# Kernel tuning notes

Hardware: AMD Instinct MI355X
Metric: run time of the kernel (lower is better)

Reference implementation:

```python
import jax, jax.numpy as jnp
import numpy as np

B, N, C = 16, 4096, 384
H_RES = W_RES = 64  # input_resolution; n == h*w
NUM_HEADS = 12
ROPE_BASE = 10000.0


def _rope_angles(h, w, c):
    # feature_dim = c, 2 channel dims -> k_max = c // 4
    k_max = c // 4
    theta = 1.0 / (ROPE_BASE ** (jnp.arange(k_max, dtype=jnp.float32) / k_max))
    hh = jnp.arange(h, dtype=jnp.float32)[:, None, None] * theta  # (h,1,k_max) -> bcast
    ww = jnp.arange(w, dtype=jnp.float32)[None, :, None] * theta  # (1,w,k_max)
    hh = jnp.broadcast_to(hh, (h, w, k_max))
    ww = jnp.broadcast_to(ww, (h, w, k_max))
    angles = jnp.concatenate([hh, ww], axis=-1)  # (h, w, c//2)
    return jnp.cos(angles), jnp.sin(angles)


def _apply_rope(x_img, cos, sin):
    # x_img: (b, h, w, c); complex rotation on (re, im) channel pairs
    b, h, w, c = x_img.shape
    xr = x_img.reshape(b, h, w, c // 2, 2)
    re, im = xr[..., 0], xr[..., 1]
    out_re = cos * re - sin * im
    out_im = sin * re + cos * im
    return jnp.stack([out_re, out_im], axis=-1).reshape(b, h, w, c)


def setup_inputs() -> dict:
    key = jax.random.key(0)
    ks = jax.random.split(key, 5)
    x = jax.random.normal(ks[0], (B, N, C), dtype=jnp.float32)
    qk_w = jax.random.normal(ks[1], (2 * C, C), dtype=jnp.float32) * (1.0 / np.sqrt(C))
    qk_b = jax.random.normal(ks[2], (2 * C,), dtype=jnp.float32) * 0.02
    lepe_w = jax.random.normal(ks[3], (C, 1, 3, 3), dtype=jnp.float32) * (1.0 / 3.0)
    lepe_b = jax.random.normal(ks[4], (C,), dtype=jnp.float32) * 0.02
    return {"x": x, "qk_w": qk_w, "qk_b": qk_b, "lepe_w": lepe_w, "lepe_b": lepe_b}


def reference(x, qk_w, qk_b, lepe_w, lepe_b):
    b, n, c = x.shape
    h = w = int(np.sqrt(n))
    nh = NUM_HEADS
    d = c // nh

    qk = x @ qk_w.T + qk_b                       # (b, n, 2c)
    q = jax.nn.elu(qk[..., :c]) + 1.0            # (b, n, c)
    k = jax.nn.elu(qk[..., c:]) + 1.0            # (b, n, c)
    v = x

    cos, sin = _rope_angles(h, w, c)             # (h, w, c//2)
    q_rope = _apply_rope(q.reshape(b, h, w, c), cos, sin).reshape(b, n, nh, d)
    k_rope = _apply_rope(k.reshape(b, h, w, c), cos, sin).reshape(b, n, nh, d)

    qh = q.reshape(b, n, nh, d)
    kh = k.reshape(b, n, nh, d)
    vh = v.reshape(b, n, nh, d)

    # z = 1 / (q . mean_n(k) + eps), per head per token
    k_mean = kh.mean(axis=1)                     # (b, nh, d)
    z = 1.0 / (jnp.einsum('bnhd,bhd->bnh', qh, k_mean) + 1e-6)  # (b, n, nh)

    # linear attention: kv = (k_rope^T v) / n ; out = q_rope @ kv
    kv = jnp.einsum('bnhd,bnhe->bhde', k_rope, vh) / n          # (b, nh, d, d)
    out = jnp.einsum('bnhd,bhde->bnhe', q_rope, kv)             # (b, n, nh, d)
    out = (out * z[..., None]).reshape(b, n, c)

    # LePE: depthwise 3x3 conv on v as image (NHWC)
    v_img = v.reshape(b, h, w, c)
    w_hwio = jnp.transpose(lepe_w, (2, 3, 1, 0))  # (3,3,1,c)
    lepe = jax.lax.conv_general_dilated(
        v_img, w_hwio, window_strides=(1, 1), padding='SAME',
        dimension_numbers=('NHWC', 'HWIO', 'NHWC'), feature_group_count=c)
    lepe = lepe + lepe_b

    return out + lepe.reshape(b, n, c)
```

## Files before the change

### kernel.cpp

```cpp
#include <hip/hip_runtime.h>

#define CDIM 384
#define NTOK 4096
#define NHEAD 12
#define KV_FLOATS (16 * NHEAD * 1024)
#define SCR_FLOATS (KV_FLOATS + 16 * CDIM)

typedef unsigned short ushort_t;
typedef __attribute__((ext_vector_type(8))) short bf16x8;
typedef __attribute__((ext_vector_type(4))) float f32x4;
typedef __attribute__((ext_vector_type(4))) unsigned short u16x4;
typedef __attribute__((ext_vector_type(8))) unsigned short u16x8;

__device__ __attribute__((aligned(16))) float g_scr[SCR_FLOATS];
__device__ __attribute__((aligned(16))) ushort_t g_xbf[(size_t)16 * 4096 * 384];
__device__ __attribute__((aligned(16))) ushort_t g_wbf[768 * 384];
__device__ __attribute__((aligned(16))) float g_part[(size_t)16 * 3 * 32 * 4096];
__device__ __attribute__((aligned(16))) float g_kspart[(size_t)16 * 3 * 32 * 256];
__device__ int g_flag;

__device__ __forceinline__ float bf2f(ushort_t u) {
  union { unsigned int i; float f; } z; z.i = ((unsigned int)u) << 16; return z.f;
}
__device__ __forceinline__ ushort_t f2bf(float f) {
  union { float f; unsigned int i; } z; z.f = f;
  unsigned int r = z.i + 0x7FFFu + ((z.i >> 16) & 1u);
  return (ushort_t)(r >> 16);
}
__device__ __forceinline__ float ldf(const void* p, size_t i, bool fp32) {
  return fp32 ? ((const float*)p)[i] : bf2f(((const ushort_t*)p)[i]);
}

__device__ __forceinline__ void load4(const void* src, size_t off, bool fp32, float o[4]) {
  if (fp32) {
    f32x4 v = *(const f32x4*)((const float*)src + off);
    o[0] = v[0]; o[1] = v[1]; o[2] = v[2]; o[3] = v[3];
  } else {
    u16x4 v = *(const u16x4*)((const ushort_t*)src + off);
    o[0] = bf2f(v[0]); o[1] = bf2f(v[1]); o[2] = bf2f(v[2]); o[3] = bf2f(v[3]);
  }
}

__device__ __forceinline__ u16x8 cvt8(const void* src, size_t off, bool fp32) {
  if (fp32) {
    const float* p = (const float*)src + off;
    f32x4 a = *(const f32x4*)p;
    f32x4 b = *(const f32x4*)(p + 4);
    u16x8 t;
    t[0] = f2bf(a[0]); t[1] = f2bf(a[1]); t[2] = f2bf(a[2]); t[3] = f2bf(a[3]);
    t[4] = f2bf(b[0]); t[5] = f2bf(b[1]); t[6] = f2bf(b[2]); t[7] = f2bf(b[3]);
    return t;
  }
  return *(const u16x8*)((const ushort_t*)src + off);
}

#define GLL16(gp, lp) __builtin_amdgcn_global_load_lds( \
    (const __attribute__((address_space(1))) unsigned int*)(const void*)(gp), \
    (__attribute__((address_space(3))) unsigned int*)(void*)(lp), 16, 0, 0)

__device__ __forceinline__ void gemm128c(const ushort_t* __restrict__ xg,
                                         const ushort_t* __restrict__ wg,
                                         ushort_t* lds, int tid, f32x4 acc[4][4])
{
  f32x4 zz = {0.f, 0.f, 0.f, 0.f};
  #pragma unroll
  for (int i = 0; i < 4; ++i)
    #pragma unroll
    for (int j = 0; j < 4; ++j) acc[i][j] = zz;

  const int lane = tid & 63, quad = lane >> 4, l15 = lane & 15;
  const int wv = tid >> 6, wm = wv >> 1, wn = wv & 1;
  const int srow = tid >> 2;
  const int sc   = tid & 3;
  const int sx   = (l15 >> 1) & 3;

  const ushort_t* xa = xg + (size_t)srow * CDIM + sc * 8;
  const ushort_t* wa = wg + (size_t)srow * CDIM + sc * 8;

  #define STAGE_STEP(buf, ks) do {                                   \
    ushort_t* la_ = lds + (buf) * 8192;                              \
    ushort_t* lb_ = la_ + 4096;                                      \
    GLL16(xa + (ks),                  la_ + tid * 8);                \
    GLL16(xa + (ks) + 64 * CDIM,      la_ + 2048 + tid * 8);         \
    GLL16(wa + (ks),                  lb_ + tid * 8);                \
    GLL16(wa + (ks) + 64 * CDIM,      lb_ + 2048 + tid * 8);         \
  } while (0)

  STAGE_STEP(0, 0);
  #pragma unroll
  for (int s = 0; s < 12; ++s) {
    const int cur = s & 1;
    if (s < 11) {
      STAGE_STEP(cur ^ 1, (s + 1) * 32);
      asm volatile("s_waitcnt vmcnt(4)" ::: "memory");
    } else {
      asm volatile("s_waitcnt vmcnt(0)" ::: "memory");
    }
    __builtin_amdgcn_s_barrier();
    asm volatile("" ::: "memory");
    const ushort_t* la = lds + cur * 8192;
    const ushort_t* lb = la + 4096;
    bf16x8 aF[4], bF[4];
    #pragma unroll
    for (int i = 0; i < 4; ++i)
      aF[i] = *(const bf16x8*)(la + (wm * 64 + l15) * 32 + i * 512 + (quad ^ sx) * 8);
    #pragma unroll
    for (int j = 0; j < 4; ++j)
      bF[j] = *(const bf16x8*)(lb + (wn * 64 + l15) * 32 + j * 512 + (quad ^ sx) * 8);
    #pragma unroll
    for (int i = 0; i < 4; ++i)
      #pragma unroll
      for (int j = 0; j < 4; ++j)
        acc[i][j] = __builtin_amdgcn_mfma_f32_16x16x32_bf16(aF[i], bF[j], acc[i][j], 0, 0, 0);
    asm volatile("" ::: "memory");
    __builtin_amdgcn_s_barrier();
  }
  #undef STAGE_STEP
}

__global__ __launch_bounds__(256) void prep(const void* __restrict__ x,
                                            const void* __restrict__ qkw) {
  __shared__ int sflag;
  const int tid = threadIdx.x;
  if (tid < 64) {
    ushort_t u = ((const ushort_t*)x)[tid];
    int e = (u >> 7) & 0xFF;
    int ok = (e >= 117 && e <= 136) ? 1 : 0;
    unsigned long long m = __ballot(ok);
    if (tid == 0) {
      int f = (__popcll(m) >= 52) ? 0 : 1;
      sflag = f;
      if (blockIdx.x == 0) g_flag = f;
    }
  }
  __syncthreads();
  const bool fp32 = (sflag != 0);
  const int gid = blockIdx.x * 256 + tid;

  if (gid < 768 * 48) {
    const int oc = gid / 48, ck = gid - oc * 48;
    u16x8 t = cvt8(qkw, (size_t)gid * 8, fp32);
    const int ckp = (ck & ~3) | ((ck & 3) ^ ((oc >> 1) & 3));
    *(u16x8*)(g_wbf + (size_t)oc * CDIM + ckp * 8) = t;
  }
  const int total = 16 * 4096 * 48;
  for (int c = gid; c < total; c += 2048 * 256) {
    const int n = c / 48, ck = c - n * 48;
    u16x8 t = cvt8(x, (size_t)c * 8, fp32);
    const int ckp = (ck & ~3) | ((ck & 3) ^ ((n >> 1) & 3));
    *(u16x8*)(g_xbf + (size_t)n * CDIM + ckp * 8) = t;
  }
}

__global__ __launch_bounds__(256) void k1(const void* __restrict__ qkb)
{
  __shared__ __align__(16) char smem[53248];
  ushort_t* xs = (ushort_t*)smem;
  ushort_t* kropeT = (ushort_t*)smem;
  ushort_t* vT = (ushort_t*)(smem + 34816);

  const bool fp32 = (g_flag != 0);
  const int tid = threadIdx.x;
  const int nt = blockIdx.x, ct = blockIdx.y, b = blockIdx.z;

  f32x4 acc[4][4];
  gemm128c(g_xbf + ((size_t)b * NTOK + (size_t)nt * 128) * CDIM,
           g_wbf + (size_t)(CDIM + ct * 128) * CDIM, xs, tid, acc);

  const int lane = tid & 63, quad = lane >> 4, l15 = lane & 15;
  const int wv = tid >> 6, wm = wv >> 1, wn = wv & 1;

  #pragma unroll
  for (int j = 0; j < 4; ++j) {
    const float bj = ldf(qkb, CDIM + ct * 128 + wn * 64 + j * 16 + l15, fp32);
    #pragma unroll
    for (int i = 0; i < 4; ++i)
      #pragma unroll
      for (int r = 0; r < 4; ++r) {
        float v = acc[i][j][r] + bj;
        acc[i][j][r] = v > 0.f ? v + 1.f : __expf(v);
      }
  }

  #pragma unroll
  for (int j = 0; j < 4; ++j) {
    float s = 0.f;
    #pragma unroll
    for (int i = 0; i < 4; ++i)
      #pragma unroll
      for (int r = 0; r < 4; ++r) s += acc[i][j][r];
    s += __shfl_down(s, 32);
    s += __shfl_down(s, 16);
    if (lane < 16)
      g_kspart[(size_t)(((b * 3 + ct) * 32 + nt) * 2 + wm) * 128 + wn * 64 + j * 16 + l15] = s;
  }

  float th[4]; bool sel[4];
  #pragma unroll
  for (int j = 0; j < 4; ++j) {
    int o = ct * 128 + wn * 64 + j * 16 + l15;
    int p = o >> 1;
    sel[j] = p < 96;
    int jj = sel[j] ? p : p - 96;
    th[j] = exp2f(-0.13841367062030676f * (float)jj);
  }
  #pragma unroll
  for (int i = 0; i < 4; ++i)
    #pragma unroll
    for (int r = 0; r < 4; ++r) {
      const int row  = wm * 64 + i * 16 + quad * 4 + r;
      const int ntok = nt * 128 + row;
      const float hhf = (float)(ntok >> 6), wwf = (float)(ntok & 63);
      #pragma unroll
      for (int j = 0; j < 4; ++j) {
        float ang = (sel[j] ? hhf : wwf) * th[j];
        float sn, cs;
        __sincosf(ang, &sn, &cs);
        float v0 = acc[i][j][r];
        float other = __shfl_xor(v0, 1);
        if (!(lane & 1)) {
          const int o = wn * 64 + j * 16 + l15;
          kropeT[o * 136 + row]       = f2bf(cs * v0 - sn * other);
          kropeT[(o + 1) * 136 + row] = f2bf(sn * v0 + cs * other);
        }
      }
    }

  const int hl = wv;
  f32x4 zz = {0.f, 0.f, 0.f, 0.f};
  f32x4 acc2[2][2];
  acc2[0][0] = zz; acc2[0][1] = zz; acc2[1][0] = zz; acc2[1][1] = zz;

  #pragma unroll
  for (int h = 0; h < 2; ++h) {
    __syncthreads();
    const int t64 = tid & 63;
    const size_t nrow = (size_t)b * NTOK + (size_t)nt * 128 + h * 64 + t64;
    #pragma unroll
    for (int it = 0; it < 4; ++it) {
      const int g = it * 4 + wv;
      const int ckt = ct * 16 + g;
      const int ckp = (ckt & ~3) | ((ckt & 3) ^ ((int)(nrow >> 1) & 3));
      u16x8 vv = *(const u16x8*)(g_xbf + nrow * CDIM + ckp * 8);
      #pragma unroll
      for (int i = 0; i < 8; ++i) vT[(g * 8 + i) * 72 + t64] = vv[i];
    }
    __syncthreads();
    #pragma unroll
    for (int ks = 0; ks < 2; ++ks) {
      bf16x8 a0 = *(const bf16x8*)(kropeT + (hl * 32 + l15) * 136      + h * 64 + ks * 32 + quad * 8);
      bf16x8 a1 = *(const bf16x8*)(kropeT + (hl * 32 + 16 + l15) * 136 + h * 64 + ks * 32 + quad * 8);
      bf16x8 b0 = *(const bf16x8*)(vT + (hl * 32 + l15) * 72      + ks * 32 + quad * 8);
      bf16x8 b1 = *(const bf16x8*)(vT + (hl * 32 + 16 + l15) * 72 + ks * 32 + quad * 8);
      acc2[0][0] = __builtin_amdgcn_mfma_f32_16x16x32_bf16(a0, b0, acc2[0][0], 0, 0, 0);
      acc2[0][1] = __builtin_amdgcn_mfma_f32_16x16x32_bf16(a0, b1, acc2[0][1], 0, 0, 0);
      acc2[1][0] = __builtin_amdgcn_mfma_f32_16x16x32_bf16(a1, b0, acc2[1][0], 0, 0, 0);
      acc2[1][1] = __builtin_amdgcn_mfma_f32_16x16x32_bf16(a1, b1, acc2[1][1], 0, 0, 0);
    }
  }

  float* dst = g_part + ((size_t)(((b * 3 + ct) * 32 + nt) * 4 + hl)) * 1024;
  #pragma unroll
  for (int mt = 0; mt < 2; ++mt)
    #pragma unroll
    for (int n2 = 0; n2 < 2; ++n2)
      #pragma unroll
      for (int r = 0; r < 4; ++r)
        dst[(mt * 16 + quad * 4 + r) * 32 + n2 * 16 + l15] = acc2[mt][n2][r];
}

__global__ __launch_bounds__(256) void red() {
  const int t = blockIdx.x * 256 + threadIdx.x;
  if (blockIdx.x < 192) {
    const int o = t * 4;
    const int b = o / 12288, r = o - b * 12288;
    const int h = r >> 10, off = r & 1023;
    const int ct = h >> 2, hl = h & 3;
    const float* p = g_part + ((size_t)((b * 3 + ct) * 32) * 4 + hl) * 1024 + off;
    f32x4 s = {0.f, 0.f, 0.f, 0.f};
    #pragma unroll 8
    for (int nt = 0; nt < 32; ++nt) {
      f32x4 v = *(const f32x4*)(p + (size_t)nt * 4096);
      s[0] += v[0]; s[1] += v[1]; s[2] += v[2]; s[3] += v[3];
    }
    *(f32x4*)(g_scr + (size_t)b * 12288 + h * 1024 + off) = s;
  } else {
    const int s4 = (t - 192 * 256) * 4;
    if (s4 < 16 * 384) {
      const int b = s4 / 384, ch = s4 - b * 384;
      const int ct = ch >> 7, chl = ch & 127;
      const float* p = g_kspart + (size_t)((b * 3 + ct) * 32) * 256 + chl;
      f32x4 s = {0.f, 0.f, 0.f, 0.f};
      #pragma unroll 8
      for (int nt = 0; nt < 32; ++nt) {
        f32x4 v0 = *(const f32x4*)(p + nt * 256);
        f32x4 v1 = *(const f32x4*)(p + nt * 256 + 128);
        s[0] += v0[0] + v1[0]; s[1] += v0[1] + v1[1];
        s[2] += v0[2] + v1[2]; s[3] += v0[3] + v1[3];
      }
      *(f32x4*)(g_scr + KV_FLOATS + (size_t)b * 384 + ch) = s;
    }
  }
}

__global__ __launch_bounds__(256) void k2(const void* __restrict__ x,
                                          const void* __restrict__ qkb,
                                          const void* __restrict__ lepw,
                                          const void* __restrict__ lepb,
                                          void* __restrict__ out)
{
  __shared__ __align__(16) char smem[50176];
  ushort_t* xs  = (ushort_t*)smem;
  ushort_t* qr  = (ushort_t*)smem;
  float* lepL = (float*)smem;
  ushort_t* kvT = (ushort_t*)(smem + 34816);
  float* zl = (float*)(smem + 43008);
  float* lw = (float*)(smem + 45056);
  float* lb = (float*)(smem + 49664);

  const bool fp32 = (g_flag != 0);
  const int tid = threadIdx.x;
  const int nt = blockIdx.x, ct = blockIdx.y, b = blockIdx.z;
  const float* kv_g   = g_scr;
  const float* ksum_g = g_scr + KV_FLOATS;

  for (int g = tid; g < 1152; g += 256) lw[g] = ldf(lepw, (size_t)ct * 1152 + g, fp32);
  if (tid < 128) lb[tid] = ldf(lepb, ct * 128 + tid, fp32);

  f32x4 acc[4][4];
  gemm128c(g_xbf + ((size_t)b * NTOK + (size_t)nt * 128) * CDIM,
           g_wbf + (size_t)(ct * 128) * CDIM, xs, tid, acc);

  const int lane = tid & 63, quad = lane >> 4, l15 = lane & 15;
  const int wv = tid >> 6, wm = wv >> 1, wn = wv & 1;

  #pragma unroll
  for (int j = 0; j < 4; ++j) {
    const float bj = ldf(qkb, ct * 128 + wn * 64 + j * 16 + l15, fp32);
    #pragma unroll
    for (int i = 0; i < 4; ++i)
      #pragma unroll
      for (int r = 0; r < 4; ++r) {
        float v = acc[i][j][r] + bj;
        acc[i][j][r] = v > 0.f ? v + 1.f : __expf(v);
      }
  }

  float km[4];
  #pragma unroll
  for (int j = 0; j < 4; ++j)
    km[j] = ksum_g[b * CDIM + ct * 128 + wn * 64 + j * 16 + l15] * (1.f / 4096.f);
  #pragma unroll
  for (int i = 0; i < 4; ++i)
    #pragma unroll
    for (int r = 0; r < 4; ++r) {
      float p0 = acc[i][0][r] * km[0] + acc[i][1][r] * km[1];
      float p1 = acc[i][2][r] * km[2] + acc[i][3][r] * km[3];
      #pragma unroll
      for (int off = 8; off > 0; off >>= 1) {
        p0 += __shfl_down(p0, off, 16);
        p1 += __shfl_down(p1, off, 16);
      }
      if (l15 == 0) {
        int row = wm * 64 + i * 16 + quad * 4 + r;
        zl[row * 4 + wn * 2]     = 1.f / (p0 + 1e-6f);
        zl[row * 4 + wn * 2 + 1] = 1.f / (p1 + 1e-6f);
      }
    }

  float th[4]; bool sel[4];
  #pragma unroll
  for (int j = 0; j < 4; ++j) {
    int o = ct * 128 + wn * 64 + j * 16 + l15;
    int p = o >> 1;
    sel[j] = p < 96;
    int jj = sel[j] ? p : p - 96;
    th[j] = exp2f(-0.13841367062030676f * (float)jj);
  }
  #pragma unroll
  for (int i = 0; i < 4; ++i)
    #pragma unroll
    for (int r = 0; r < 4; ++r) {
      const int row  = wm * 64 + i * 16 + quad * 4 + r;
      const int ntok = nt * 128 + row;
      const float hhf = (float)(ntok >> 6), wwf = (float)(ntok & 63);
      #pragma unroll
      for (int j = 0; j < 4; ++j) {
        float ang = (sel[j] ? hhf : wwf) * th[j];
        float sn, cs;
        __sincosf(ang, &sn, &cs);
        float v0 = acc[i][j][r];
        float other = __shfl_xor(v0, 1);
        if (!(lane & 1)) {
          ushort2 t = make_ushort2(f2bf(cs * v0 - sn * other), f2bf(sn * v0 + cs * other));
          *(ushort2*)(qr + row * 136 + wn * 64 + j * 16 + l15) = t;
        }
      }
    }

  const float* kvb = kv_g + (size_t)(b * NHEAD + ct * 4) * 1024;
  #pragma unroll
  for (int s = 0; s < 16; ++s) {
    int g = s * 256 + tid;
    int hl2 = g >> 10, dd = (g >> 5) & 31, e = g & 31;
    kvT[hl2 * 1024 + e * 32 + dd] = f2bf(kvb[g] * (1.f / 4096.f));
  }
  __syncthreads();

  const int hl = tid >> 6;
  bf16x8 aF[8];
  #pragma unroll
  for (int i = 0; i < 8; ++i)
    aF[i] = *(const bf16x8*)(qr + (i * 16 + l15) * 136 + hl * 32 + quad * 8);
  __syncthreads();

  const int cc  = tid & 31;
  const int ch4 = cc * 4;
  const int gg  = tid >> 5;
  const int w0  = gg * 8;
  const float lbv0 = lb[ch4], lbv1 = lb[ch4 + 1], lbv2 = lb[ch4 + 2], lbv3 = lb[ch4 + 3];

  #pragma unroll
  for (int h = 0; h < 2; ++h) {
    if (h) __syncthreads();

    f32x4 zzv = {0.f, 0.f, 0.f, 0.f};
    f32x4 oac4[4][2];
    #pragma unroll
    for (int iloc = 0; iloc < 4; ++iloc) { oac4[iloc][0] = zzv; oac4[iloc][1] = zzv; }
    #pragma unroll
    for (int jn = 0; jn < 2; ++jn) {
      bf16x8 bF = *(const bf16x8*)(kvT + hl * 1024 + (jn * 16 + l15) * 32 + quad * 8);
      #pragma unroll
      for (int iloc = 0; iloc < 4; ++iloc)
        oac4[iloc][jn] = __builtin_amdgcn_mfma_f32_16x16x32_bf16(aF[h * 4 + iloc], bF, oac4[iloc][jn], 0, 0, 0);
    }
    #pragma unroll
    for (int iloc = 0; iloc < 4; ++iloc)
      #pragma unroll
      for (int jn = 0; jn < 2; ++jn)
        #pragma unroll
        for (int r = 0; r < 4; ++r) {
          const int rowloc = iloc * 16 + quad * 4 + r;
          lepL[rowloc * 132 + hl * 32 + jn * 16 + l15] =
              oac4[iloc][jn][r] * zl[(h * 64 + rowloc) * 4 + hl];
        }
    __syncthreads();

    const int hh = nt * 2 + h;
    float accv[8][4];
    #pragma unroll
    for (int s = 0; s < 8; ++s) {
      accv[s][0] = lbv0; accv[s][1] = lbv1; accv[s][2] = lbv2; accv[s][3] = lbv3;
    }
    #pragma unroll
    for (int rk = 0; rk < 3; ++rk) {
      const int ih = hh + rk - 1;
      if ((unsigned)ih < 64u) {
        float wr0[4], wr1[4], wr2[4];
        #pragma unroll
        for (int c = 0; c < 4; ++c) {
          wr0[c] = lw[(ch4 + c) * 9 + rk * 3 + 0];
          wr1[c] = lw[(ch4 + c) * 9 + rk * 3 + 1];
          wr2[c] = lw[(ch4 + c) * 9 + rk * 3 + 2];
        }
        const size_t rowbase = ((size_t)b * NTOK + (size_t)(ih * 64)) * CDIM
                             + (size_t)ct * 128 + ch4;
        float av[4], bv[4], cv[4];
        if (w0 > 0) load4(x, rowbase + (size_t)(w0 - 1) * CDIM, fp32, av);
        else { av[0] = av[1] = av[2] = av[3] = 0.f; }
        load4(x, rowbase + (size_t)w0 * CDIM, fp32, bv);
        #pragma unroll
        for (int s = 0; s < 8; ++s) {
          const int iwn = w0 + s + 1;
          if (iwn < 64) load4(x, rowbase + (size_t)iwn * CDIM, fp32, cv);
          else { cv[0] = cv[1] = cv[2] = cv[3] = 0.f; }
          #pragma unroll
          for (int c = 0; c < 4; ++c)
            accv[s][c] += wr0[c] * av[c] + wr1[c] * bv[c] + wr2[c] * cv[c];
          #pragma unroll
          for (int c = 0; c < 4; ++c) { av[c] = bv[c]; bv[c] = cv[c]; }
        }
      }
    }
    #pragma unroll
    for (int s = 0; s < 8; ++s) {
      f32x4 a = *(const f32x4*)(lepL + (w0 + s) * 132 + ch4);
      float r0 = accv[s][0] + a[0];
      float r1 = accv[s][1] + a[1];
      float r2 = accv[s][2] + a[2];
      float r3 = accv[s][3] + a[3];
      const size_t oi = ((size_t)b * NTOK + (size_t)(nt * 128 + h * 64 + w0 + s)) * CDIM
                      + (size_t)ct * 128 + ch4;
      if (fp32) {
        f32x4 t; t[0] = r0; t[1] = r1; t[2] = r2; t[3] = r3;
        *(f32x4*)((float*)out + oi) = t;
      } else {
        u16x4 t; t[0] = f2bf(r0); t[1] = f2bf(r1); t[2] = f2bf(r2); t[3] = f2bf(r3);
        *(u16x4*)((ushort_t*)out + oi) = t;
      }
    }
  }
}

extern "C" void kernel_launch(void* const* d_in, const int* in_sizes, int n_in,
                              void* d_out, int out_size, void* d_ws, size_t ws_size,
                              hipStream_t stream) {
  const void* x    = d_in[0];
  const void* qkw  = d_in[1];
  const void* qkb  = d_in[2];
  const void* lepw = d_in[3];
  const void* lepb = d_in[4];

  prep<<<2048, 256, 0, stream>>>(x, qkw);
  dim3 grid(32, 3, 16), blk(256, 1, 1);
  k1<<<grid, blk, 0, stream>>>(qkb);
  red<<<198, 256, 0, stream>>>();
  k2<<<grid, blk, 0, stream>>>(x, qkb, lepw, lepb, d_out);
}
```

Baseline: 356.0 us.

## Read LePE input from bf16 copy, hoist row RoPE sincos, pad kvT LDS

```diff
diff --git a/kernel.cpp b/kernel.cpp
--- a/kernel.cpp
+++ b/kernel.cpp
@@ -31,14 +31,12 @@
   return fp32 ? ((const float*)p)[i] : bf2f(((const ushort_t*)p)[i]);
 }
 
-__device__ __forceinline__ void load4(const void* src, size_t off, bool fp32, float o[4]) {
-  if (fp32) {
-    f32x4 v = *(const f32x4*)((const float*)src + off);
-    o[0] = v[0]; o[1] = v[1]; o[2] = v[2]; o[3] = v[3];
-  } else {
-    u16x4 v = *(const u16x4*)((const ushort_t*)src + off);
-    o[0] = bf2f(v[0]); o[1] = bf2f(v[1]); o[2] = bf2f(v[2]); o[3] = bf2f(v[3]);
-  }
+__device__ __forceinline__ void load4b(const ushort_t* xbb, int n, int ct, int ch4, float o[4]) {
+  const int ckt = ct * 16 + (ch4 >> 3);
+  const int ckp = (ckt & ~3) | ((ckt & 3) ^ ((n >> 1) & 3));
+  const ushort_t* p = xbb + (size_t)n * CDIM + ckp * 8 + (ch4 & 7);
+  u16x4 v = *(const u16x4*)p;
+  o[0] = bf2f(v[0]); o[1] = bf2f(v[1]); o[2] = bf2f(v[2]); o[3] = bf2f(v[3]);
 }
 
 __device__ __forceinline__ u16x8 cvt8(const void* src, size_t off, bool fp32) {
@@ -195,7 +193,8 @@
       g_kspart[(size_t)(((b * 3 + ct) * 32 + nt) * 2 + wm) * 128 + wn * 64 + j * 16 + l15] = s;
   }
 
-  float th[4]; bool sel[4];
+  float th[4]; bool sel[4]; float hsn[4], hcs[4];
+  const float hhf = (float)(nt * 2 + wm);
   #pragma unroll
   for (int j = 0; j < 4; ++j) {
     int o = ct * 128 + wn * 64 + j * 16 + l15;
@@ -203,19 +202,19 @@
     sel[j] = p < 96;
     int jj = sel[j] ? p : p - 96;
     th[j] = exp2f(-0.13841367062030676f * (float)jj);
+    if (sel[j]) __sincosf(hhf * th[j], &hsn[j], &hcs[j]);
   }
   #pragma unroll
   for (int i = 0; i < 4; ++i)
     #pragma unroll
     for (int r = 0; r < 4; ++r) {
-      const int row  = wm * 64 + i * 16 + quad * 4 + r;
-      const int ntok = nt * 128 + row;
-      const float hhf = (float)(ntok >> 6), wwf = (float)(ntok & 63);
+      const int row = wm * 64 + i * 16 + quad * 4 + r;
+      const float wwf = (float)(i * 16 + quad * 4 + r);
       #pragma unroll
       for (int j = 0; j < 4; ++j) {
-        float ang = (sel[j] ? hhf : wwf) * th[j];
         float sn, cs;
-        __sincosf(ang, &sn, &cs);
+        if (sel[j]) { sn = hsn[j]; cs = hcs[j]; }
+        else        __sincosf(wwf * th[j], &sn, &cs);
         float v0 = acc[i][j][r];
         float other = __shfl_xor(v0, 1);
         if (!(lane & 1)) {
@@ -303,26 +302,26 @@
   }
 }
 
-__global__ __launch_bounds__(256) void k2(const void* __restrict__ x,
-                                          const void* __restrict__ qkb,
+__global__ __launch_bounds__(256) void k2(const void* __restrict__ qkb,
                                           const void* __restrict__ lepw,
                                           const void* __restrict__ lepb,
                                           void* __restrict__ out)
 {
-  __shared__ __align__(16) char smem[50176];
+  __shared__ __align__(16) char smem[52224];
   ushort_t* xs  = (ushort_t*)smem;
   ushort_t* qr  = (ushort_t*)smem;
   float* lepL = (float*)smem;
   ushort_t* kvT = (ushort_t*)(smem + 34816);
-  float* zl = (float*)(smem + 43008);
-  float* lw = (float*)(smem + 45056);
-  float* lb = (float*)(smem + 49664);
+  float* zl = (float*)(smem + 45056);
+  float* lw = (float*)(smem + 47104);
+  float* lb = (float*)(smem + 51712);
 
   const bool fp32 = (g_flag != 0);
   const int tid = threadIdx.x;
   const int nt = blockIdx.x, ct = blockIdx.y, b = blockIdx.z;
   const float* kv_g   = g_scr;
   const float* ksum_g = g_scr + KV_FLOATS;
+  const ushort_t* xbb = g_xbf + (size_t)b * NTOK * CDIM;
 
   for (int g = tid; g < 1152; g += 256) lw[g] = ldf(lepw, (size_t)ct * 1152 + g, fp32);
   if (tid < 128) lb[tid] = ldf(lepb, ct * 128 + tid, fp32);
@@ -368,7 +367,8 @@
       }
     }
 
-  float th[4]; bool sel[4];
+  float th[4]; bool sel[4]; float hsn[4], hcs[4];
+  const float hhf = (float)(nt * 2 + wm);
   #pragma unroll
   for (int j = 0; j < 4; ++j) {
     int o = ct * 128 + wn * 64 + j * 16 + l15;
@@ -376,19 +376,19 @@
     sel[j] = p < 96;
     int jj = sel[j] ? p : p - 96;
     th[j] = exp2f(-0.13841367062030676f * (float)jj);
+    if (sel[j]) __sincosf(hhf * th[j], &hsn[j], &hcs[j]);
   }
   #pragma unroll
   for (int i = 0; i < 4; ++i)
     #pragma unroll
     for (int r = 0; r < 4; ++r) {
-      const int row  = wm * 64 + i * 16 + quad * 4 + r;
-      const int ntok = nt * 128 + row;
-      const float hhf = (float)(ntok >> 6), wwf = (float)(ntok & 63);
+      const int row = wm * 64 + i * 16 + quad * 4 + r;
+      const float wwf = (float)(i * 16 + quad * 4 + r);
       #pragma unroll
       for (int j = 0; j < 4; ++j) {
-        float ang = (sel[j] ? hhf : wwf) * th[j];
         float sn, cs;
-        __sincosf(ang, &sn, &cs);
+        if (sel[j]) { sn = hsn[j]; cs = hcs[j]; }
+        else        __sincosf(wwf * th[j], &sn, &cs);
         float v0 = acc[i][j][r];
         float other = __shfl_xor(v0, 1);
         if (!(lane & 1)) {
@@ -403,7 +403,7 @@
   for (int s = 0; s < 16; ++s) {
     int g = s * 256 + tid;
     int hl2 = g >> 10, dd = (g >> 5) & 31, e = g & 31;
-    kvT[hl2 * 1024 + e * 32 + dd] = f2bf(kvb[g] * (1.f / 4096.f));
+    kvT[hl2 * 1280 + e * 40 + dd] = f2bf(kvb[g] * (1.f / 4096.f));
   }
   __syncthreads();
 
@@ -430,7 +430,7 @@
     for (int iloc = 0; iloc < 4; ++iloc) { oac4[iloc][0] = zzv; oac4[iloc][1] = zzv; }
     #pragma unroll
     for (int jn = 0; jn < 2; ++jn) {
-      bf16x8 bF = *(const bf16x8*)(kvT + hl * 1024 + (jn * 16 + l15) * 32 + quad * 8);
+      bf16x8 bF = *(const bf16x8*)(kvT + hl * 1280 + (jn * 16 + l15) * 40 + quad * 8);
       #pragma unroll
       for (int iloc = 0; iloc < 4; ++iloc)
         oac4[iloc][jn] = __builtin_amdgcn_mfma_f32_16x16x32_bf16(aF[h * 4 + iloc], bF, oac4[iloc][jn], 0, 0, 0);
@@ -464,16 +464,15 @@
           wr1[c] = lw[(ch4 + c) * 9 + rk * 3 + 1];
           wr2[c] = lw[(ch4 + c) * 9 + rk * 3 + 2];
         }
-        const size_t rowbase = ((size_t)b * NTOK + (size_t)(ih * 64)) * CDIM
-                             + (size_t)ct * 128 + ch4;
+        const int tokbase = ih * 64;
         float av[4], bv[4], cv[4];
-        if (w0 > 0) load4(x, rowbase + (size_t)(w0 - 1) * CDIM, fp32, av);
+        if (w0 > 0) load4b(xbb, tokbase + w0 - 1, ct, ch4, av);
         else { av[0] = av[1] = av[2] = av[3] = 0.f; }
-        load4(x, rowbase + (size_t)w0 * CDIM, fp32, bv);
+        load4b(xbb, tokbase + w0, ct, ch4, bv);
         #pragma unroll
         for (int s = 0; s < 8; ++s) {
           const int iwn = w0 + s + 1;
-          if (iwn < 64) load4(x, rowbase + (size_t)iwn * CDIM, fp32, cv);
+          if (iwn < 64) load4b(xbb, tokbase + iwn, ct, ch4, cv);
           else { cv[0] = cv[1] = cv[2] = cv[3] = 0.f; }
           #pragma unroll
           for (int c = 0; c < 4; ++c)
@@ -516,5 +515,5 @@
   dim3 grid(32, 3, 16), blk(256, 1, 1);
   k1<<<grid, blk, 0, stream>>>(qkb);
   red<<<198, 256, 0, stream>>>();
-  k2<<<grid, blk, 0, stream>>>(x, qkb, lepw, lepb, d_out);
-}
+  k2<<<grid, blk, 0, stream>>>(qkb, lepw, lepb, d_out);
+}
```

Measured after the change: 379.9 us. +6.7%, slower.
